# Kernel optimization log

Hardware: AMD Instinct MI355X
Metric: run time of the kernel (lower is better)

## Reference

```python
import jax, jax.numpy as jnp
import numpy as np

DIM = 96
D_STATE = 16
EXPAND = 2
D_INNER = EXPAND * DIM
DT_RANK = (DIM + 15) // 16  # 6
B, H, W = 2, 64, 64
K = 4  # scan directions


def _ln(x, w, b, eps=1e-5):
    mu = x.mean(-1, keepdims=True)
    var = x.var(-1, keepdims=True)
    return (x - mu) / jnp.sqrt(var + eps) * w + b


def setup_inputs() -> dict:
    key = jax.random.key(0)
    ks = jax.random.split(key, 10)
    f = jnp.float32
    x = jax.random.normal(ks[0], (B, H, W, DIM), dtype=f)
    y = jax.random.normal(ks[1], (B, H, W, DIM), dtype=f)
    inp = {
        'x': x,
        'y': y,
        'ln_w': jnp.ones((DIM,), f),
        'ln_b': jnp.zeros((DIM,), f),
        'in_proj_w': jax.random.normal(ks[2], (2 * D_INNER, DIM), f) * 0.05,
        'conv_w': jax.random.normal(ks[3], (D_INNER, 1, 3, 3), f) * 0.1,
        'conv_b': jnp.zeros((D_INNER,), f),
        'x_proj_w': jax.random.normal(ks[4], (K, DT_RANK + 2 * D_STATE, D_INNER), f) * 0.05,
        'dt_w': jax.random.normal(ks[5], (K, D_INNER, DT_RANK), f) * 0.1,
        'dt_b': jax.random.normal(ks[6], (K, D_INNER), f) * 0.1,
        'A_log': jnp.broadcast_to(jnp.log(jnp.arange(1, D_STATE + 1, dtype=f)), (K, D_INNER, D_STATE)),
        'Ds': jnp.ones((K, D_INNER), f),
        'out_norm_w': jnp.ones((D_INNER,), f),
        'out_norm_b': jnp.zeros((D_INNER,), f),
        'out_proj_w': jax.random.normal(ks[7], (DIM, D_INNER), f) * 0.05,
    }
    return inp


def _fwd(x, y, ln_w, ln_b, in_proj_w, conv_w, conv_b, x_proj_w, dt_w, dt_b,
         A_log, Ds, out_norm_w, out_norm_b, out_proj_w):
    Bsz, Hh, Ww, C = x.shape
    Din = conv_w.shape[0]
    N = A_log.shape[-1]
    R = dt_w.shape[-1]
    L = Hh * Ww

    diff = jnp.abs(x - y)                       # TemporalSpectrumBlock abs-diff
    h = _ln(diff, ln_w, ln_b)                   # VSSBlock ln_1
    xz = h @ in_proj_w.T                        # (B,H,W,2*Din)
    xm, z = jnp.split(xz, 2, axis=-1)
    xm = xm.transpose(0, 3, 1, 2)               # (B,Din,H,W)
    xm = jax.lax.conv_general_dilated(
        xm, conv_w, (1, 1), 'SAME', feature_group_count=Din,
        dimension_numbers=('NCHW', 'OIHW', 'NCHW')) + conv_b[None, :, None, None]
    xm = jax.nn.silu(xm)

    # 4-directional sequences (B,4,Din,L)
    x0 = xm.reshape(Bsz, Din, L)
    x1 = xm.transpose(0, 1, 3, 2).reshape(Bsz, Din, L)
    xs = jnp.stack([x0, x1], axis=1)
    xs = jnp.concatenate([xs, jnp.flip(xs, axis=-1)], axis=1)

    x_dbl = jnp.einsum('bkdl,kcd->bkcl', xs, x_proj_w)
    dts, Bs, Cs = jnp.split(x_dbl, [R, R + N], axis=2)   # (B,4,R,L),(B,4,N,L),(B,4,N,L)
    dts = jnp.einsum('bkrl,kdr->bkdl', dts, dt_w)
    delta = jax.nn.softplus(dts + dt_b[None, :, :, None])  # (B,4,Din,L)

    A = -jnp.exp(A_log)                                    # (4,Din,N)
    dA = jnp.exp(delta[..., None] * A[None, :, :, None, :])          # (B,4,Din,L,N)
    dBu = delta[..., None] * Bs.transpose(0, 1, 3, 2)[:, :, None] * xs[..., None]

    dA_t = dA.transpose(3, 0, 1, 2, 4)    # (L,B,4,Din,N)
    dBu_t = dBu.transpose(3, 0, 1, 2, 4)
    C_t = Cs.transpose(3, 0, 1, 2)        # (L,B,4,N)
    h0 = jnp.zeros((Bsz, 4, Din, N), dtype=x.dtype)

    def step(hc, inp):
        a, bu, c = inp
        hc = a * hc + bu
        yv = jnp.einsum('bkdn,bkn->bkd', hc, c)
        return hc, yv

    _, ys = jax.lax.scan(step, h0, (dA_t, dBu_t, C_t))    # (L,B,4,Din)
    ys = ys.transpose(1, 2, 3, 0)                          # (B,4,Din,L)
    out_y = ys + Ds[None, :, :, None] * xs

    inv_y = jnp.flip(out_y[:, 2:4], axis=-1)
    wh_y = out_y[:, 1].reshape(Bsz, Din, Ww, Hh).transpose(0, 1, 3, 2).reshape(Bsz, Din, L)
    invwh_y = inv_y[:, 1].reshape(Bsz, Din, Ww, Hh).transpose(0, 1, 3, 2).reshape(Bsz, Din, L)
    yc = out_y[:, 0] + inv_y[:, 0] + wh_y + invwh_y        # (B,Din,L)
    yc = yc.transpose(0, 2, 1).reshape(Bsz, Hh, Ww, Din)

    yn = _ln(yc, out_norm_w, out_norm_b)
    out = (yn * jax.nn.silu(z)) @ out_proj_w.T
    return diff + out                                      # residual around the block


def reference(x, y, ln_w, ln_b, in_proj_w, conv_w, conv_b, x_proj_w, dt_w, dt_b,
              A_log, Ds, out_norm_w, out_norm_b, out_proj_w):
    return _fwd(x, y, ln_w, ln_b, in_proj_w, conv_w, conv_b, x_proj_w, dt_w, dt_b,
                A_log, Ds, out_norm_w, out_norm_b, out_proj_w)
```

## Files before the change

### kernel.cpp

```cpp
#include <hip/hip_runtime.h>
#include <math.h>

#define DIMC 96
#define DIN  192
#define NST  16
#define RNK  6
#define KD   4
#define HH   64
#define WWD  64
#define LL   4096
#define BB   2
#define NC   256
#define LOG_NC 8
#define CH   16
#define CPK  48

__device__ __forceinline__ int pos_of(int k, int l) {
    int t = ((l & 63) << 6) | (l >> 6);
    switch (k) {
        case 0: return l;
        case 1: return t;
        case 2: return LL - 1 - l;
        default: return ((((LL-1-l) & 63) << 6) | ((LL-1-l) >> 6));
    }
}

__device__ __forceinline__ float silu_f(float v) {
    return v / (1.f + __expf(-v));
}

__global__ __launch_bounds__(256) void k0_prep(
    const float* __restrict__ Win, const float* __restrict__ Wout,
    const float* __restrict__ xpw,
    float* __restrict__ WinT, float* __restrict__ WoutT, float* __restrict__ wT3)
{
    int idx = blockIdx.x*256 + threadIdx.x;
    int stride = gridDim.x*256;
    for (int i = idx; i < 96*384; i += stride) {
        int j = i / 384, o = i - j*384;
        WinT[i] = Win[o*96 + j];
    }
    for (int i = idx; i < 192*96; i += stride) {
        int j = i / 96, o = i - j*96;
        WoutT[i] = Wout[o*192 + j];
    }
    for (int i = idx; i < KD*192*CPK; i += stride) {
        int kk = i / (192*CPK); int rem = i - kk*192*CPK;
        int j = rem / CPK, c = rem - j*CPK;
        float v = 0.f;
        if (c < 16)       v = xpw[((size_t)kk*(RNK+2*NST) + RNK + c)*DIN + j];
        else if (c < 32)  v = xpw[((size_t)kk*(RNK+2*NST) + RNK + NST + (c-16))*DIN + j];
        else if (c < 38)  v = xpw[((size_t)kk*(RNK+2*NST) + (c-32))*DIN + j];
        wT3[i] = v;
    }
}

__global__ __launch_bounds__(1024) void k1_ln_inproj(
    const float* __restrict__ x, const float* __restrict__ y,
    const float* __restrict__ lnw, const float* __restrict__ lnb,
    const float* __restrict__ WinT,
    float* __restrict__ diff, float* __restrict__ xm, float* __restrict__ zbuf)
{
    __shared__ float hT[96*65];
    __shared__ float ps1[16*64], ps2[16*64];
    __shared__ float mus[64], rss[64];
    int t = threadIdx.x;
    int ptile = blockIdx.x >> 1, cgrp = blockIdx.x & 1;
    int p0 = ptile*64;

    #pragma unroll
    for (int s = 0; s < 6; s++) {
        int i = t + 1024*s;
        float v = fabsf(x[(size_t)p0*96 + i] - y[(size_t)p0*96 + i]);
        if (cgrp == 0) diff[(size_t)p0*96 + i] = v;
        int pos = i / 96, ch = i - pos*96;
        hT[ch*65 + pos] = v;
    }
    __syncthreads();
    {
        int pos = t & 63, part = t >> 6;
        float s1 = 0.f, s2 = 0.f;
        #pragma unroll
        for (int m = 0; m < 6; m++) {
            float v = hT[(part*6 + m)*65 + pos];
            s1 += v; s2 += v*v;
        }
        ps1[part*64 + pos] = s1; ps2[part*64 + pos] = s2;
    }
    __syncthreads();
    if (t < 64) {
        float S1 = 0.f, S2 = 0.f;
        #pragma unroll
        for (int i = 0; i < 16; i++) { S1 += ps1[i*64 + t]; S2 += ps2[i*64 + t]; }
        float mu = S1 * (1.f/96.f);
        float var = S2 * (1.f/96.f) - mu*mu;
        mus[t] = mu; rss[t] = rsqrtf(var + 1e-5f);
    }
    __syncthreads();
    #pragma unroll
    for (int s = 0; s < 6; s++) {
        int i = t + 1024*s;
        int pos = i / 96, ch = i - pos*96;
        hT[ch*65 + pos] = (hT[ch*65 + pos] - mus[pos]) * rss[pos] * lnw[ch] + lnb[ch];
    }
    __syncthreads();

    int w = __builtin_amdgcn_readfirstlane(t >> 6);
    int lane = t & 63;
    int c0 = cgrp*192 + w*12;
    const float* wp = WinT + c0;
    float acc[12];
    #pragma unroll
    for (int cc = 0; cc < 12; cc++) acc[cc] = 0.f;
    #pragma unroll 2
    for (int j = 0; j < 96; j++) {
        float u = hT[j*65 + lane];
        const float* wrow = wp + j*384;
        #pragma unroll
        for (int cc = 0; cc < 12; cc++) acc[cc] += u * wrow[cc];
    }
    size_t p = (size_t)(p0 + lane);
    float* dst = (c0 < 192) ? (xm + p*192 + c0) : (zbuf + p*192 + (c0 - 192));
    #pragma unroll
    for (int q = 0; q < 3; q++)
        *(float4*)&dst[4*q] = make_float4(acc[4*q], acc[4*q+1], acc[4*q+2], acc[4*q+3]);
}

__global__ __launch_bounds__(192) void k2_conv(
    const float* __restrict__ xm, const float* __restrict__ cw,
    const float* __restrict__ cb, float* __restrict__ xconv)
{
    int p = blockIdx.x;
    int d = threadIdx.x;
    int b = p >> 12;
    int l = p & (LL - 1);
    int hh = l >> 6, ww = l & 63;
    float acc = cb[d];
    const float* wd = cw + d*9;
    #pragma unroll
    for (int di = -1; di <= 1; di++) {
        int h2 = hh + di;
        if ((unsigned)h2 < HH) {
            #pragma unroll
            for (int dj = -1; dj <= 1; dj++) {
                int w2 = ww + dj;
                if ((unsigned)w2 < WWD)
                    acc += wd[(di+1)*3 + (dj+1)] * xm[((size_t)b*LL + h2*WWD + w2)*DIN + d];
            }
        }
    }
    xconv[(size_t)p*DIN + d] = silu_f(acc);
}

__global__ __launch_bounds__(512) void k3_xproj(
    const float* __restrict__ xconv, const float* __restrict__ wT3,
    float* __restrict__ XDK)
{
    __shared__ float uT[64*192];
    int t = threadIdx.x;
    int ptile = blockIdx.x >> 1, wgrp = blockIdx.x & 1;
    int p0 = ptile*64;

    #pragma unroll
    for (int s = 0; s < 24; s++) {
        int i = t + 512*s;
        int pos = i / 192, ch = i - pos*192;
        int c4 = (ch >> 2) ^ (pos & 7);
        uT[pos*192 + (c4 << 2) + (ch & 3)] = xconv[(size_t)(p0 + pos)*192 + ch];
    }
    __syncthreads();

    int w = __builtin_amdgcn_readfirstlane(t >> 6);
    int slot = wgrp*8 + w;
    int k = slot >> 2, cq = slot & 3;
    int lane = t & 63;
    int c0 = cq*12;
    const float* wp = wT3 + (size_t)k*192*CPK + c0;
    const float* urow = uT + lane*192;
    int sw = lane & 7;
    float acc[12];
    #pragma unroll
    for (int cc = 0; cc < 12; cc++) acc[cc] = 0.f;
    #pragma unroll 4
    for (int j4 = 0; j4 < 48; j4++) {
        float4 u4 = *(const float4*)&urow[((j4 ^ sw) << 2)];
        const float* wrow = wp + (j4*4)*CPK;
        #pragma unroll
        for (int cc = 0; cc < 12; cc++) acc[cc] += u4.x * wrow[cc];
        #pragma unroll
        for (int cc = 0; cc < 12; cc++) acc[cc] += u4.y * wrow[CPK + cc];
        #pragma unroll
        for (int cc = 0; cc < 12; cc++) acc[cc] += u4.z * wrow[2*CPK + cc];
        #pragma unroll
        for (int cc = 0; cc < 12; cc++) acc[cc] += u4.w * wrow[3*CPK + cc];
    }
    int p = p0 + lane;
    int b = p >> 12;
    int s = p & (LL - 1);
    int ts = ((s & 63) << 6) | (s >> 6);
    int l;
    switch (k) {
        case 0: l = s; break;
        case 1: l = ts; break;
        case 2: l = LL - 1 - s; break;
        default: l = LL - 1 - ts; break;
    }
    float* dst = XDK + ((size_t)(b*KD + k)*LL + l)*CPK + c0;
    #pragma unroll
    for (int q = 0; q < 3; q++)
        *(float4*)&dst[4*q] = make_float4(acc[4*q], acc[4*q+1], acc[4*q+2], acc[4*q+3]);
}

__global__ __launch_bounds__(192) void k4_scanA(
    const float* __restrict__ xconv, const float* __restrict__ XDK,
    const float* __restrict__ dtw, const float* __restrict__ dtb,
    const float* __restrict__ A_log,
    float* __restrict__ Sarr, float* __restrict__ Q)
{
    int blk = blockIdx.x;
    int c  = blk & (NC - 1);
    int bk = blk >> LOG_NC;
    int k  = bk & 3;
    int b  = bk >> 2;
    int d  = threadIdx.x;
    float dw[RNK];
    #pragma unroll
    for (int r = 0; r < RNK; r++) dw[r] = dtw[((size_t)k*DIN + d)*RNK + r];
    float bias = dtb[k*DIN + d];
    float A[NST];
    #pragma unroll
    for (int n = 0; n < NST; n++) A[n] = -__expf(A_log[((size_t)k*DIN + d)*NST + n]);
    bool fastA = true;
    #pragma unroll
    for (int n = 1; n < NST; n++)
        fastA = fastA && (fabsf(A[n] - (float)(n+1)*A[0]) <= 1e-4f*(float)(n+1));

    float h[NST];
    #pragma unroll
    for (int n = 0; n < NST; n++) h[n] = 0.f;
    float S = 0.f;

    size_t rb = ((size_t)bk*LL + c*CH)*CPK;
    if (fastA) {
        #pragma unroll 2
        for (int step = 0; step < CH; step++) {
            const float* rec = XDK + rb + step*CPK;
            float dl = bias;
            #pragma unroll
            for (int r = 0; r < RNK; r++) dl += rec[32 + r] * dw[r];
            dl = (dl > 20.f) ? dl : __logf(1.f + __expf(dl));
            int l = c*CH + step;
            float uu = xconv[((size_t)b*LL + pos_of(k, l))*DIN + d];
            float du = dl * uu;
            S += dl;
            float e1 = __expf(dl * A[0]);
            float e2 = e1*e1, e4 = e2*e2;
            float p0 = e1, p1 = e2, p2 = e2*e1, p3 = e4;
            #pragma unroll
            for (int g = 0; g < 4; g++) {
                h[4*g+0] = p0*h[4*g+0] + du*rec[4*g+0];
                h[4*g+1] = p1*h[4*g+1] + du*rec[4*g+1];
                h[4*g+2] = p2*h[4*g+2] + du*rec[4*g+2];
                h[4*g+3] = p3*h[4*g+3] + du*rec[4*g+3];
                if (g < 3) { p0 *= e4; p1 *= e4; p2 *= e4; p3 *= e4; }
            }
        }
    } else {
        #pragma unroll 2
        for (int step = 0; step < CH; step++) {
            const float* rec = XDK + rb + step*CPK;
            float dl = bias;
            #pragma unroll
            for (int r = 0; r < RNK; r++) dl += rec[32 + r] * dw[r];
            dl = (dl > 20.f) ? dl : __logf(1.f + __expf(dl));
            int l = c*CH + step;
            float uu = xconv[((size_t)b*LL + pos_of(k, l))*DIN + d];
            float du = dl * uu;
            S += dl;
            #pragma unroll
            for (int n = 0; n < NST; n++) {
                float a = __expf(dl * A[n]);
                h[n] = a*h[n] + du*rec[n];
            }
        }
    }
    Sarr[(size_t)blk*DIN + d] = S;
    size_t qb = (size_t)blk*NST*DIN + d;
    #pragma unroll
    for (int n = 0; n < NST; n++) Q[qb + n*DIN] = h[n];
}

__global__ __launch_bounds__(256) void k5_scanB(
    const float* __restrict__ A_log, const float* __restrict__ Sarr,
    float* __restrict__ Q)
{
    int idx = blockIdx.x*256 + threadIdx.x;
    if (idx >= BB*KD*NST*DIN) return;
    int d = idx % DIN;
    int rest = idx / DIN;
    int n = rest % NST; rest /= NST;
    int k = rest & 3;
    int b = rest >> 2;
    int bk = b*KD + k;
    float A = -__expf(A_log[((size_t)k*DIN + d)*NST + n]);
    size_t qstride = (size_t)NST*DIN;
    size_t qbase = (size_t)bk*NC*qstride + n*DIN + d;
    size_t sbase = (size_t)bk*NC*DIN + d;
    float h = 0.f;
    #pragma unroll 4
    for (int c = 0; c < NC; c++) {
        float s = Sarr[sbase + c*DIN];
        float q = Q[qbase + c*qstride];
        Q[qbase + c*qstride] = h;
        h = __expf(A*s)*h + q;
    }
}

__global__ __launch_bounds__(192) void k6_scanC(
    const float* __restrict__ xconv, const float* __restrict__ XDK,
    const float* __restrict__ dtw, const float* __restrict__ dtb,
    const float* __restrict__ A_log, const float* __restrict__ Ds,
    const float* __restrict__ Q, float* __restrict__ outy)
{
    int blk = blockIdx.x;
    int c  = blk & (NC - 1);
    int bk = blk >> LOG_NC;
    int k  = bk & 3;
    int b  = bk >> 2;
    int d  = threadIdx.x;
    float dw[RNK];
    #pragma unroll
    for (int r = 0; r < RNK; r++) dw[r] = dtw[((size_t)k*DIN + d)*RNK + r];
    float bias = dtb[k*DIN + d];
    float A[NST];
    #pragma unroll
    for (int n = 0; n < NST; n++) A[n] = -__expf(A_log[((size_t)k*DIN + d)*NST + n]);
    bool fastA = true;
    #pragma unroll
    for (int n = 1; n < NST; n++)
        fastA = fastA && (fabsf(A[n] - (float)(n+1)*A[0]) <= 1e-4f*(float)(n+1));
    float h[NST];
    size_t qb = (size_t)blk*NST*DIN + d;
    #pragma unroll
    for (int n = 0; n < NST; n++) h[n] = Q[qb + n*DIN];
    float Dv = Ds[k*DIN + d];

    size_t rb = ((size_t)bk*LL + c*CH)*CPK;
    if (fastA) {
        #pragma unroll 2
        for (int step = 0; step < CH; step++) {
            const float* rec = XDK + rb + step*CPK;
            float dl = bias;
            #pragma unroll
            for (int r = 0; r < RNK; r++) dl += rec[32 + r] * dw[r];
            dl = (dl > 20.f) ? dl : __logf(1.f + __expf(dl));
            int l = c*CH + step;
            int sp = pos_of(k, l);
            float uu = xconv[((size_t)b*LL + sp)*DIN + d];
            float du = dl * uu;
            float e1 = __expf(dl * A[0]);
            float e2 = e1*e1, e4 = e2*e2;
            float p0 = e1, p1 = e2, p2 = e2*e1, p3 = e4;
            float yv = 0.f;
            #pragma unroll
            for (int g = 0; g < 4; g++) {
                h[4*g+0] = p0*h[4*g+0] + du*rec[4*g+0];
                h[4*g+1] = p1*h[4*g+1] + du*rec[4*g+1];
                h[4*g+2] = p2*h[4*g+2] + du*rec[4*g+2];
                h[4*g+3] = p3*h[4*g+3] + du*rec[4*g+3];
                yv += h[4*g+0]*rec[16+4*g+0] + h[4*g+1]*rec[16+4*g+1]
                    + h[4*g+2]*rec[16+4*g+2] + h[4*g+3]*rec[16+4*g+3];
                if (g < 3) { p0 *= e4; p1 *= e4; p2 *= e4; p3 *= e4; }
            }
            outy[((size_t)bk*LL + sp)*DIN + d] = yv + Dv*uu;
        }
    } else {
        #pragma unroll 2
        for (int step = 0; step < CH; step++) {
            const float* rec = XDK + rb + step*CPK;
            float dl = bias;
            #pragma unroll
            for (int r = 0; r < RNK; r++) dl += rec[32 + r] * dw[r];
            dl = (dl > 20.f) ? dl : __logf(1.f + __expf(dl));
            int l = c*CH + step;
            int sp = pos_of(k, l);
            float uu = xconv[((size_t)b*LL + sp)*DIN + d];
            float du = dl * uu;
            float yv = 0.f;
            #pragma unroll
            for (int n = 0; n < NST; n++) {
                float a = __expf(dl * A[n]);
                h[n] = a*h[n] + du*rec[n];
                yv += h[n] * rec[16 + n];
            }
            outy[((size_t)bk*LL + sp)*DIN + d] = yv + Dv*uu;
        }
    }
}

__global__ __launch_bounds__(256) void k7_out(
    const float* __restrict__ outy, const float* __restrict__ zbuf,
    const float* __restrict__ diff, const float* __restrict__ onw,
    const float* __restrict__ onb, const float* __restrict__ WoutT,
    float* __restrict__ out)
{
    __shared__ float gT[192*65];
    __shared__ float ps1[4*64], ps2[4*64];
    __shared__ float mus[64], rss[64];
    int t = threadIdx.x;
    int ptile = blockIdx.x >> 1, chalf = blockIdx.x & 1;
    int p0 = ptile*64;
    int b = p0 >> 12;
    int l0 = p0 & (LL - 1);
    const size_t seg = (size_t)LL*DIN;
    size_t base = ((size_t)(b*KD)*LL + l0)*DIN;

    #pragma unroll
    for (int s = 0; s < 48; s++) {
        int i = t + 256*s;
        float yc = outy[base + i] + outy[base + seg + i]
                 + outy[base + 2*seg + i] + outy[base + 3*seg + i];
        int pos = i / 192, ch = i - pos*192;
        gT[ch*65 + pos] = yc;
    }
    __syncthreads();
    {
        int pos = t & 63, part = t >> 6;
        float s1 = 0.f, s2 = 0.f;
        #pragma unroll
        for (int m = 0; m < 48; m++) {
            float v = gT[(part*48 + m)*65 + pos];
            s1 += v; s2 += v*v;
        }
        ps1[part*64 + pos] = s1; ps2[part*64 + pos] = s2;
    }
    __syncthreads();
    if (t < 64) {
        float S1 = ps1[t] + ps1[64+t] + ps1[128+t] + ps1[192+t];
        float S2 = ps2[t] + ps2[64+t] + ps2[128+t] + ps2[192+t];
        float mu = S1 * (1.f/192.f);
        float var = S2 * (1.f/192.f) - mu*mu;
        mus[t] = mu; rss[t] = rsqrtf(var + 1e-5f);
    }
    __syncthreads();
    #pragma unroll
    for (int s = 0; s < 48; s++) {
        int i = t + 256*s;
        int pos = i / 192, ch = i - pos*192;
        float v = gT[ch*65 + pos];
        float yn = (v - mus[pos]) * rss[pos] * onw[ch] + onb[ch];
        float z = zbuf[(size_t)p0*DIN + i];
        gT[ch*65 + pos] = yn * silu_f(z);
    }
    __syncthreads();

    int w = __builtin_amdgcn_readfirstlane(t >> 6);
    int lane = t & 63;
    int c0 = chalf*48 + w*12;
    const float* wp = WoutT + c0;
    float acc[12];
    #pragma unroll
    for (int cc = 0; cc < 12; cc++) acc[cc] = 0.f;
    #pragma unroll 2
    for (int j = 0; j < 192; j++) {
        float u = gT[j*65 + lane];
        const float* wrow = wp + j*96;
        #pragma unroll
        for (int cc = 0; cc < 12; cc++) acc[cc] += u * wrow[cc];
    }
    size_t p = (size_t)(p0 + lane);
    #pragma unroll
    for (int q = 0; q < 3; q++) {
        float4 dv = *(const float4*)&diff[p*96 + c0 + 4*q];
        *(float4*)&out[p*96 + c0 + 4*q] =
            make_float4(acc[4*q] + dv.x, acc[4*q+1] + dv.y, acc[4*q+2] + dv.z, acc[4*q+3] + dv.w);
    }
}

extern "C" void kernel_launch(void* const* d_in, const int* in_sizes, int n_in,
                              void* d_out, int out_size, void* d_ws, size_t ws_size,
                              hipStream_t stream)
{
    const float* x       = (const float*)d_in[0];
    const float* y       = (const float*)d_in[1];
    const float* ln_w    = (const float*)d_in[2];
    const float* ln_b    = (const float*)d_in[3];
    const float* in_proj = (const float*)d_in[4];
    const float* conv_w  = (const float*)d_in[5];
    const float* conv_b  = (const float*)d_in[6];
    const float* x_proj  = (const float*)d_in[7];
    const float* dt_w    = (const float*)d_in[8];
    const float* dt_b    = (const float*)d_in[9];
    const float* A_log   = (const float*)d_in[10];
    const float* Ds      = (const float*)d_in[11];
    const float* onw     = (const float*)d_in[12];
    const float* onb     = (const float*)d_in[13];
    const float* out_w   = (const float*)d_in[14];
    float* out = (float*)d_out;

    float* ws    = (float*)d_ws;
    float* diff  = ws;
    float* zbuf  = diff  + 786432;
    float* xm    = zbuf  + 1572864;
    float* xconv = xm    + 1572864;
    float* XDK   = xconv + 1572864;
    float* outy  = XDK   + 1572864;
    float* Qbuf  = outy  + 6291456;
    float* Sarr  = Qbuf  + 6291456;
    float* WinT  = Sarr  + 393216;
    float* WoutT = WinT  + 36864;
    float* wT3   = WoutT + 18432;

    const int BL = BB * LL;

    hipLaunchKernelGGL(k0_prep, dim3(144), dim3(256), 0, stream,
                       in_proj, out_w, x_proj, WinT, WoutT, wT3);
    hipLaunchKernelGGL(k1_ln_inproj, dim3(BL/64*2), dim3(1024), 0, stream,
                       x, y, ln_w, ln_b, WinT, diff, xm, zbuf);
    hipLaunchKernelGGL(k2_conv, dim3(BL), dim3(DIN), 0, stream,
                       xm, conv_w, conv_b, xconv);
    hipLaunchKernelGGL(k3_xproj, dim3(BL/64*2), dim3(512), 0, stream,
                       xconv, wT3, XDK);
    hipLaunchKernelGGL(k4_scanA, dim3(BB*KD*NC), dim3(DIN), 0, stream,
                       xconv, XDK, dt_w, dt_b, A_log, Sarr, Qbuf);
    hipLaunchKernelGGL(k5_scanB, dim3((BB*KD*NST*DIN + 255)/256), dim3(256), 0, stream,
                       A_log, Sarr, Qbuf);
    hipLaunchKernelGGL(k6_scanC, dim3(BB*KD*NC), dim3(DIN), 0, stream,
                       xconv, XDK, dt_w, dt_b, A_log, Ds, Qbuf, outy);
    hipLaunchKernelGGL(k7_out, dim3(BL/64*2), dim3(256), 0, stream,
                       outy, zbuf, diff, onw, onb, WoutT, out);
}
```

Measured before the change: 278.6 us.

## Fold weight prep into LN/in-proj kernel and halve scan chunk count

Removes the separate weight-transpose prep kernel: in_proj weights are now read directly in their original layout, and the x_proj and out_proj transposes are done by spare threads at the start of the LN/in-proj kernel. It also changes the chunked scan from 256 chunks of 16 to 128 chunks of 32, halving the grid of the scan kernels and the carry-propagation work. The direct in_proj reads are strided per output channel, which may coalesce worse, and longer chunks lengthen the serial work per block.

```diff
diff --git a/kernel.cpp b/kernel.cpp
--- a/kernel.cpp
+++ b/kernel.cpp
@@ -10,9 +10,8 @@
 #define WWD  64
 #define LL   4096
 #define BB   2
-#define NC   256
-#define LOG_NC 8
-#define CH   16
+#define NC   128
+#define CH   32
 #define CPK  48
 
 __device__ __forceinline__ int pos_of(int k, int l) {
@@ -29,37 +28,13 @@
     return v / (1.f + __expf(-v));
 }
 
-__global__ __launch_bounds__(256) void k0_prep(
-    const float* __restrict__ Win, const float* __restrict__ Wout,
-    const float* __restrict__ xpw,
-    float* __restrict__ WinT, float* __restrict__ WoutT, float* __restrict__ wT3)
-{
-    int idx = blockIdx.x*256 + threadIdx.x;
-    int stride = gridDim.x*256;
-    for (int i = idx; i < 96*384; i += stride) {
-        int j = i / 384, o = i - j*384;
-        WinT[i] = Win[o*96 + j];
-    }
-    for (int i = idx; i < 192*96; i += stride) {
-        int j = i / 96, o = i - j*96;
-        WoutT[i] = Wout[o*192 + j];
-    }
-    for (int i = idx; i < KD*192*CPK; i += stride) {
-        int kk = i / (192*CPK); int rem = i - kk*192*CPK;
-        int j = rem / CPK, c = rem - j*CPK;
-        float v = 0.f;
-        if (c < 16)       v = xpw[((size_t)kk*(RNK+2*NST) + RNK + c)*DIN + j];
-        else if (c < 32)  v = xpw[((size_t)kk*(RNK+2*NST) + RNK + NST + (c-16))*DIN + j];
-        else if (c < 38)  v = xpw[((size_t)kk*(RNK+2*NST) + (c-32))*DIN + j];
-        wT3[i] = v;
-    }
-}
-
 __global__ __launch_bounds__(1024) void k1_ln_inproj(
     const float* __restrict__ x, const float* __restrict__ y,
     const float* __restrict__ lnw, const float* __restrict__ lnb,
-    const float* __restrict__ WinT,
-    float* __restrict__ diff, float* __restrict__ xm, float* __restrict__ zbuf)
+    const float* __restrict__ Win, const float* __restrict__ Wout,
+    const float* __restrict__ xpw,
+    float* __restrict__ diff, float* __restrict__ xm, float* __restrict__ zbuf,
+    float* __restrict__ wT3, float* __restrict__ WoutT)
 {
     __shared__ float hT[96*65];
     __shared__ float ps1[16*64], ps2[16*64];
@@ -68,6 +43,23 @@
     int ptile = blockIdx.x >> 1, cgrp = blockIdx.x & 1;
     int p0 = ptile*64;
 
+    {
+        int gid = blockIdx.x*1024 + t;
+        if (gid < KD*192*CPK) {
+            int kk = gid / (192*CPK); int rem = gid - kk*192*CPK;
+            int j = rem / CPK, c = rem - j*CPK;
+            float v = 0.f;
+            if (c < 16)       v = xpw[((size_t)kk*(RNK+2*NST) + RNK + c)*DIN + j];
+            else if (c < 32)  v = xpw[((size_t)kk*(RNK+2*NST) + RNK + NST + (c-16))*DIN + j];
+            else if (c < 38)  v = xpw[((size_t)kk*(RNK+2*NST) + (c-32))*DIN + j];
+            wT3[gid] = v;
+        } else if (gid < KD*192*CPK + 192*96) {
+            int i = gid - KD*192*CPK;
+            int j = i / 96, o = i - j*96;
+            WoutT[i] = Wout[o*192 + j];
+        }
+    }
+
     #pragma unroll
     for (int s = 0; s < 6; s++) {
         int i = t + 1024*s;
@@ -108,16 +100,15 @@
     int w = __builtin_amdgcn_readfirstlane(t >> 6);
     int lane = t & 63;
     int c0 = cgrp*192 + w*12;
-    const float* wp = WinT + c0;
+    const float* wrows = Win + (size_t)c0*96;
     float acc[12];
     #pragma unroll
     for (int cc = 0; cc < 12; cc++) acc[cc] = 0.f;
     #pragma unroll 2
     for (int j = 0; j < 96; j++) {
         float u = hT[j*65 + lane];
-        const float* wrow = wp + j*384;
-        #pragma unroll
-        for (int cc = 0; cc < 12; cc++) acc[cc] += u * wrow[cc];
+        #pragma unroll
+        for (int cc = 0; cc < 12; cc++) acc[cc] += u * wrows[cc*96 + j];
     }
     size_t p = (size_t)(p0 + lane);
     float* dst = (c0 < 192) ? (xm + p*192 + c0) : (zbuf + p*192 + (c0 - 192));
@@ -219,7 +210,7 @@
 {
     int blk = blockIdx.x;
     int c  = blk & (NC - 1);
-    int bk = blk >> LOG_NC;
+    int bk = blk >> 7;
     int k  = bk & 3;
     int b  = bk >> 2;
     int d  = threadIdx.x;
@@ -324,7 +315,7 @@
 {
     int blk = blockIdx.x;
     int c  = blk & (NC - 1);
-    int bk = blk >> LOG_NC;
+    int bk = blk >> 7;
     int k  = bk & 3;
     int b  = bk >> 2;
     int d  = threadIdx.x;
@@ -507,16 +498,14 @@
     float* outy  = XDK   + 1572864;
     float* Qbuf  = outy  + 6291456;
     float* Sarr  = Qbuf  + 6291456;
-    float* WinT  = Sarr  + 393216;
-    float* WoutT = WinT  + 36864;
+    float* WoutT = Sarr  + 393216;
     float* wT3   = WoutT + 18432;
 
     const int BL = BB * LL;
 
-    hipLaunchKernelGGL(k0_prep, dim3(144), dim3(256), 0, stream,
-                       in_proj, out_w, x_proj, WinT, WoutT, wT3);
     hipLaunchKernelGGL(k1_ln_inproj, dim3(BL/64*2), dim3(1024), 0, stream,
-                       x, y, ln_w, ln_b, WinT, diff, xm, zbuf);
+                       x, y, ln_w, ln_b, in_proj, out_w, x_proj,
+                       diff, xm, zbuf, wT3, WoutT);
     hipLaunchKernelGGL(k2_conv, dim3(BL), dim3(DIN), 0, stream,
                        xm, conv_w, conv_b, xconv);
     hipLaunchKernelGGL(k3_xproj, dim3(BL/64*2), dim3(512), 0, stream,
```

Result: faster. 269.0 us (-3.4%).
